# Kernel tuning notes

Measured on AMD Instinct MI355X. Metric: run time of the kernel, lower is better.

The kernel has to match this reference:

```python
import jax, jax.numpy as jnp
import numpy as np

SEQ, BATCH, HIDDEN = 4096, 16, 512


def setup_inputs() -> dict:
    key = jax.random.key(0)
    ks = jax.random.split(key, 8)
    scale = 1.0 / np.sqrt(HIDDEN)
    outputs_hidden = jax.random.normal(ks[0], (1, BATCH, HIDDEN), jnp.float32)
    encoder_out = jax.random.normal(ks[1], (SEQ, BATCH, HIDDEN), jnp.float32)
    encoder_features = jax.random.normal(ks[2], (SEQ, BATCH, HIDDEN), jnp.float32)
    # binary-ish float mask, mostly ones
    encoder_mask = (jax.random.uniform(ks[3], (BATCH, 1, SEQ)) > 0.1).astype(jnp.float32)
    # running sum of positive exp-scores; keep strictly positive
    temporal_scores_sum = jax.random.uniform(ks[4], (BATCH, 1, SEQ)) + 0.5
    W_feat = jax.random.normal(ks[5], (HIDDEN, HIDDEN), jnp.float32) * scale
    b_feat = jax.random.normal(ks[6], (HIDDEN,), jnp.float32)
    v_attn = jax.random.normal(ks[7], (HIDDEN,), jnp.float32) * scale
    return {
        "outputs_hidden": outputs_hidden,
        "encoder_out": encoder_out,
        "encoder_features": encoder_features,
        "encoder_mask": encoder_mask,
        "temporal_scores_sum": temporal_scores_sum,
        "W_feat": W_feat,
        "b_feat": b_feat,
        "v_attn": v_attn,
    }


def reference(outputs_hidden, encoder_out, encoder_features, encoder_mask,
              temporal_scores_sum, W_feat, b_feat, v_attn):
    # self.features: Linear(hidden, hidden) on decoder state [1, b, h]
    decoder_features = jnp.einsum('obh,kh->obk', outputs_hidden, W_feat) + b_feat
    # additive score: tanh(dec + enc) . v  -> [s, b]
    scores = jnp.einsum('sbh,h->sb', jnp.tanh(decoder_features + encoder_features), v_attn)
    # Permute(1,2,0) of [s,b,1] -> [b,1,s], then exp
    temporal_attention = jnp.exp(scores).T[:, None, :]  # [b, 1, s]
    attention = temporal_attention / temporal_scores_sum
    new_scores_sum = temporal_attention + temporal_scores_sum
    attention = attention * encoder_mask
    attention = attention / jnp.sum(attention, axis=-1, keepdims=True)  # Normalize(-1)
    enc = jnp.transpose(encoder_out, (1, 0, 2))           # [b, s, h]
    context = jnp.matmul(attention, enc)                  # [b, 1, h]
    context = jnp.transpose(context, (1, 0, 2))           # [1, b, h]
    return context, attention, new_scores_sum
```

## Files before the change

kernel.cpp:

```cpp
#include <hip/hip_runtime.h>
#include <hip/hip_bf16.h>
#include <stdint.h>

#define SEQ 4096
#define BATCH 16
#define HID 512
#define ATT_OFF (BATCH * HID)
#define NSS_OFF (BATCH * HID + BATCH * SEQ)
#define SPB 16
#define NCHUNK (SEQ / SPB)
#define SPW (SPB / 4)

typedef unsigned short u16;
typedef unsigned int u32;

__device__ __forceinline__ float bflo(u32 w) { return __uint_as_float(w << 16); }
__device__ __forceinline__ float bfhi(u32 w) { return __uint_as_float(w & 0xffff0000u); }

__device__ __forceinline__ u16 f2bf(float f) {
  u32 u = __float_as_uint(f);
  return (u16)((u + 0x7fffu + ((u >> 16) & 1u)) >> 16);
}

__device__ __forceinline__ int probe_bf16(const void* tssp) {
  const u16* t = (const u16*)tssp;
  int ok = 1;
  #pragma unroll
  for (int i = 0; i < 8; i += 2) {
    u16 u = t[i];
    ok &= (u >= 0x3F00 && u <= 0x3FC0) ? 1 : 0;
  }
  return ok;
}

template <int BF>
__device__ __forceinline__ float ld1(const void* p, size_t i) {
  if (BF) return __uint_as_float(((u32)((const u16*)p)[i]) << 16);
  return ((const float*)p)[i];
}

template <int BF>
__device__ __forceinline__ void st1(void* p, size_t i, float v) {
  if (BF) ((u16*)p)[i] = f2bf(v);
  else    ((float*)p)[i] = v;
}

template <int BF>
__device__ __forceinline__ void load8(const void* p, size_t e, float* o) {
  if (BF) {
    uint4 v = *(const uint4*)((const u16*)p + e);
    o[0]=bflo(v.x); o[1]=bfhi(v.x); o[2]=bflo(v.y); o[3]=bfhi(v.y);
    o[4]=bflo(v.z); o[5]=bfhi(v.z); o[6]=bflo(v.w); o[7]=bfhi(v.w);
  } else {
    const float4* f = (const float4*)((const float*)p + e);
    float4 a = f[0], b = f[1];
    o[0]=a.x; o[1]=a.y; o[2]=a.z; o[3]=a.w;
    o[4]=b.x; o[5]=b.y; o[6]=b.z; o[7]=b.w;
  }
}

__device__ __forceinline__ float fast_tanh(float x) {
  float e = __expf(2.0f * x);
  return 1.0f - 2.0f * __builtin_amdgcn_rcpf(e + 1.0f);
}

template <int BF>
__device__ __forceinline__ void k_dec_body(
    const void* oh, const void* W, const void* bias, float* dec) {
  int tid = threadIdx.x;
  int gw = blockIdx.x * 4 + (tid >> 6);
  int lane = tid & 63;
  int k = gw & (HID - 1);
  int b = gw >> 9;
  float wv[8], ov[8];
  load8<BF>(W,  (size_t)k * HID + lane * 8, wv);
  load8<BF>(oh, (size_t)b * HID + lane * 8, ov);
  float acc = 0.0f;
  #pragma unroll
  for (int j = 0; j < 8; ++j) acc += wv[j] * ov[j];
  #pragma unroll
  for (int off = 32; off; off >>= 1) acc += __shfl_xor(acc, off, 64);
  if (lane == 0) dec[b * HID + k] = acc + ld1<BF>(bias, k);
}

__global__ __launch_bounds__(256) void k_dec(
    const void* oh, const void* W, const void* bias, const void* tss,
    float* dec, float* denom) {
  if (blockIdx.x == 0 && threadIdx.x < BATCH) denom[threadIdx.x] = 0.0f;
  if (probe_bf16(tss)) k_dec_body<1>(oh, W, bias, dec);
  else                 k_dec_body<0>(oh, W, bias, dec);
}

template <int BF>
__device__ __forceinline__ void k_scores_body(
    const void* ef, const void* maskp, const void* tssp, const void* vp,
    const float* dec, float* w_buf, float* denom, void* out) {
  int tid = threadIdx.x, lane = tid & 63, wave = tid >> 6;
  int blk = blockIdx.x;
  int b = blk & (BATCH - 1);
  int chunk = blk >> 4;
  int s0 = chunk * SPB + wave * SPW;

  float ev[SPW][8];
  #pragma unroll
  for (int i = 0; i < SPW; ++i)
    load8<BF>(ef, ((size_t)(s0 + i) * BATCH + b) * HID + lane * 8, ev[i]);

  float dv[8], vv[8];
  #pragma unroll
  for (int j = 0; j < 8; ++j) dv[j] = dec[b * HID + lane * 8 + j];
  load8<BF>(vp, lane * 8, vv);

  float acc[SPW];
  #pragma unroll
  for (int i = 0; i < SPW; ++i) {
    float s = 0.0f;
    #pragma unroll
    for (int j = 0; j < 8; ++j) s += fast_tanh(ev[i][j] + dv[j]) * vv[j];
    acc[i] = s;
  }
  #pragma unroll
  for (int off = 32; off; off >>= 1) {
    #pragma unroll
    for (int i = 0; i < SPW; ++i) acc[i] += __shfl_xor(acc[i], off, 64);
  }
  float wsum = 0.0f;
  #pragma unroll
  for (int i = 0; i < SPW; ++i) {
    int s = s0 + i;
    float p  = __expf(acc[i]);
    float ts = ld1<BF>(tssp,  b * SEQ + s);
    float m  = ld1<BF>(maskp, b * SEQ + s);
    float wv = p * m * __builtin_amdgcn_rcpf(ts);
    wsum += wv;
    if (lane == 0) {
      st1<BF>(out, NSS_OFF + b * SEQ + s, p + ts);
      w_buf[b * SEQ + s] = wv;
    }
  }
  __shared__ float wpart[4];
  if (lane == 0) wpart[wave] = wsum;
  __syncthreads();
  if (tid == 0)
    atomicAdd(&denom[b], wpart[0] + wpart[1] + wpart[2] + wpart[3]);
}

__global__ __launch_bounds__(256, 4) void k_scores(
    const void* ef, const void* maskp, const void* tssp, const void* vp,
    const float* dec, float* w_buf, float* denom, void* out) {
  if (probe_bf16(tssp))
    k_scores_body<1>(ef, maskp, tssp, vp, dec, w_buf, denom, out);
  else
    k_scores_body<0>(ef, maskp, tssp, vp, dec, w_buf, denom, out);
}

template <int BF>
__device__ __forceinline__ void k_ctx_body(
    const void* eo, const float* w_buf, float* partial) {
  int tid = threadIdx.x, lane = tid & 63, wave = tid >> 6;
  int blk = blockIdx.x;
  int b = blk & (BATCH - 1);
  int chunk = blk >> 4;
  int s0 = chunk * SPB + wave * SPW;

  float eov[SPW][8];
  #pragma unroll
  for (int i = 0; i < SPW; ++i)
    load8<BF>(eo, ((size_t)(s0 + i) * BATCH + b) * HID + lane * 8, eov[i]);

  float w[SPW];
  #pragma unroll
  for (int i = 0; i < SPW; ++i) w[i] = w_buf[b * SEQ + s0 + i];

  float a[8] = {0,0,0,0,0,0,0,0};
  #pragma unroll
  for (int i = 0; i < SPW; ++i)
    #pragma unroll
    for (int j = 0; j < 8; ++j) a[j] += w[i] * eov[i][j];

  __shared__ float red[3 * 8 * 64];
  if (wave > 0) {
    #pragma unroll
    for (int j = 0; j < 8; ++j) red[((wave - 1) * 8 + j) * 64 + lane] = a[j];
  }
  __syncthreads();
  if (wave == 0) {
    #pragma unroll
    for (int k = 0; k < 3; ++k)
      #pragma unroll
      for (int j = 0; j < 8; ++j) a[j] += red[(k * 8 + j) * 64 + lane];
    float4* p4 = (float4*)(partial + ((size_t)b * NCHUNK + chunk) * HID + lane * 8);
    p4[0] = make_float4(a[0], a[1], a[2], a[3]);
    p4[1] = make_float4(a[4], a[5], a[6], a[7]);
  }
}

__global__ __launch_bounds__(256, 4) void k_ctx(
    const void* eo, const void* tssp, const float* w_buf, float* partial) {
  if (probe_bf16(tssp)) k_ctx_body<1>(eo, w_buf, partial);
  else                  k_ctx_body<0>(eo, w_buf, partial);
}

template <int BF>
__device__ __forceinline__ void k_fin_body(
    const float* w_buf, const float* denom, const float* partial, void* out) {
  int b = blockIdx.x >> 5;
  int part = blockIdx.x & 31;
  int t = threadIdx.x;
  float inv_d = __builtin_amdgcn_rcpf(denom[b]);
  if (t < 128) {
    int s = part * 128 + t;
    st1<BF>(out, ATT_OFF + b * SEQ + s, w_buf[b * SEQ + s] * inv_d);
  }
  int hl = t >> 4, cp = t & 15;
  int h = part * 16 + hl;
  float sum = 0.0f;
  #pragma unroll
  for (int c = cp; c < NCHUNK; c += 16)
    sum += partial[((size_t)b * NCHUNK + c) * HID + h];
  #pragma unroll
  for (int off = 8; off; off >>= 1) sum += __shfl_xor(sum, off, 64);
  if (cp == 0) st1<BF>(out, b * HID + h, sum * inv_d);
}

__global__ __launch_bounds__(256) void k_finalize(
    const float* w_buf, const float* denom, const float* partial,
    const void* tssp, void* out) {
  if (probe_bf16(tssp)) k_fin_body<1>(w_buf, denom, partial, out);
  else                  k_fin_body<0>(w_buf, denom, partial, out);
}

extern "C" void kernel_launch(void* const* d_in, const int* in_sizes, int n_in,
                              void* d_out, int out_size, void* d_ws, size_t ws_size,
                              hipStream_t stream) {
  const void* oh   = d_in[0];
  const void* eo   = d_in[1];
  const void* ef   = d_in[2];
  const void* mask = d_in[3];
  const void* tss  = d_in[4];
  const void* W    = d_in[5];
  const void* bias = d_in[6];
  const void* v    = d_in[7];

  float* ws      = (float*)d_ws;
  float* dec     = ws;
  float* w_buf   = dec + BATCH * HID;
  float* denom   = w_buf + BATCH * SEQ;
  float* partial = denom + 16;

  k_dec     <<<2048, 256, 0, stream>>>(oh, W, bias, tss, dec, denom);
  k_scores  <<<4096, 256, 0, stream>>>(ef, mask, tss, v, dec, w_buf, denom, d_out);
  k_ctx     <<<4096, 256, 0, stream>>>(eo, tss, w_buf, partial);
  k_finalize<<< 512, 256, 0, stream>>>(w_buf, denom, partial, tss, d_out);
}
```

Before: 322.4 us.

## Software-pipeline streaming kernels with double-buffered tiles and fewer, larger blocks

The scores and context kernels now have each wave handle four tiles of four sequence positions, using two register buffers. The next tile's loads are issued before the current tile is computed, so memory latency overlaps with compute. The grid shrinks fourfold, which means fewer atomics on the denominator and fewer partial rows for finalize to reduce. The cost is higher register pressure, so occupancy is lowered to 3 blocks per SIMD, and there are fewer blocks available to hide latency.

```diff
diff --git a/kernel.cpp b/kernel.cpp
--- a/kernel.cpp
+++ b/kernel.cpp
@@ -7,9 +7,12 @@
 #define HID 512
 #define ATT_OFF (BATCH * HID)
 #define NSS_OFF (BATCH * HID + BATCH * SEQ)
-#define SPB 16
-#define NCHUNK (SEQ / SPB)
-#define SPW (SPB / 4)
+
+#define SPW 4
+#define NT 4
+#define SBLK (4 * NT * SPW)
+#define NGRP (SEQ / SBLK)
+#define NSTREAM_BLOCKS (BATCH * NGRP)
 
 typedef unsigned short u16;
 typedef unsigned int u32;
@@ -98,46 +101,64 @@
   int tid = threadIdx.x, lane = tid & 63, wave = tid >> 6;
   int blk = blockIdx.x;
   int b = blk & (BATCH - 1);
-  int chunk = blk >> 4;
-  int s0 = chunk * SPB + wave * SPW;
-
-  float ev[SPW][8];
-  #pragma unroll
-  for (int i = 0; i < SPW; ++i)
-    load8<BF>(ef, ((size_t)(s0 + i) * BATCH + b) * HID + lane * 8, ev[i]);
+  int grp = blk >> 4;
+  int sw = grp * SBLK + wave * (NT * SPW);
 
   float dv[8], vv[8];
   #pragma unroll
   for (int j = 0; j < 8; ++j) dv[j] = dec[b * HID + lane * 8 + j];
   load8<BF>(vp, lane * 8, vv);
 
-  float acc[SPW];
-  #pragma unroll
-  for (int i = 0; i < SPW; ++i) {
-    float s = 0.0f;
-    #pragma unroll
-    for (int j = 0; j < 8; ++j) s += fast_tanh(ev[i][j] + dv[j]) * vv[j];
-    acc[i] = s;
-  }
-  #pragma unroll
-  for (int off = 32; off; off >>= 1) {
-    #pragma unroll
-    for (int i = 0; i < SPW; ++i) acc[i] += __shfl_xor(acc[i], off, 64);
-  }
+  float evA[SPW][8], evB[SPW][8];
+  float tsA[SPW], tsB[SPW], mA[SPW], mB[SPW];
   float wsum = 0.0f;
-  #pragma unroll
-  for (int i = 0; i < SPW; ++i) {
-    int s = s0 + i;
-    float p  = __expf(acc[i]);
-    float ts = ld1<BF>(tssp,  b * SEQ + s);
-    float m  = ld1<BF>(maskp, b * SEQ + s);
-    float wv = p * m * __builtin_amdgcn_rcpf(ts);
-    wsum += wv;
-    if (lane == 0) {
-      st1<BF>(out, NSS_OFF + b * SEQ + s, p + ts);
-      w_buf[b * SEQ + s] = wv;
-    }
-  }
+
+  auto LOADT = [&](float (&buf)[SPW][8], float (&ts)[SPW], float (&m)[SPW],
+                   int t) {
+    int s0 = sw + t * SPW;
+    #pragma unroll
+    for (int i = 0; i < SPW; ++i)
+      load8<BF>(ef, ((size_t)(s0 + i) * BATCH + b) * HID + lane * 8, buf[i]);
+    #pragma unroll
+    for (int i = 0; i < SPW; ++i) {
+      ts[i] = ld1<BF>(tssp,  b * SEQ + s0 + i);
+      m[i]  = ld1<BF>(maskp, b * SEQ + s0 + i);
+    }
+  };
+  auto COMP = [&](float (&buf)[SPW][8], float (&ts)[SPW], float (&m)[SPW],
+                  int t) {
+    int s0 = sw + t * SPW;
+    float acc[SPW];
+    #pragma unroll
+    for (int i = 0; i < SPW; ++i) {
+      float s = 0.0f;
+      #pragma unroll
+      for (int j = 0; j < 8; ++j) s += fast_tanh(buf[i][j] + dv[j]) * vv[j];
+      acc[i] = s;
+    }
+    #pragma unroll
+    for (int off = 32; off; off >>= 1) {
+      #pragma unroll
+      for (int i = 0; i < SPW; ++i) acc[i] += __shfl_xor(acc[i], off, 64);
+    }
+    #pragma unroll
+    for (int i = 0; i < SPW; ++i) {
+      float p  = __expf(acc[i]);
+      float wv = p * m[i] * __builtin_amdgcn_rcpf(ts[i]);
+      wsum += wv;
+      if (lane == 0) {
+        st1<BF>(out, NSS_OFF + b * SEQ + s0 + i, p + ts[i]);
+        w_buf[b * SEQ + s0 + i] = wv;
+      }
+    }
+  };
+
+  LOADT(evA, tsA, mA, 0);
+  LOADT(evB, tsB, mB, 1);  COMP(evA, tsA, mA, 0);
+  LOADT(evA, tsA, mA, 2);  COMP(evB, tsB, mB, 1);
+  LOADT(evB, tsB, mB, 3);  COMP(evA, tsA, mA, 2);
+                           COMP(evB, tsB, mB, 3);
+
   __shared__ float wpart[4];
   if (lane == 0) wpart[wave] = wsum;
   __syncthreads();
@@ -145,7 +166,7 @@
     atomicAdd(&denom[b], wpart[0] + wpart[1] + wpart[2] + wpart[3]);
 }
 
-__global__ __launch_bounds__(256, 4) void k_scores(
+__global__ __launch_bounds__(256, 3) void k_scores(
     const void* ef, const void* maskp, const void* tssp, const void* vp,
     const float* dec, float* w_buf, float* denom, void* out) {
   if (probe_bf16(tssp))
@@ -160,23 +181,33 @@
   int tid = threadIdx.x, lane = tid & 63, wave = tid >> 6;
   int blk = blockIdx.x;
   int b = blk & (BATCH - 1);
-  int chunk = blk >> 4;
-  int s0 = chunk * SPB + wave * SPW;
-
-  float eov[SPW][8];
-  #pragma unroll
-  for (int i = 0; i < SPW; ++i)
-    load8<BF>(eo, ((size_t)(s0 + i) * BATCH + b) * HID + lane * 8, eov[i]);
-
-  float w[SPW];
-  #pragma unroll
-  for (int i = 0; i < SPW; ++i) w[i] = w_buf[b * SEQ + s0 + i];
-
+  int grp = blk >> 4;
+  int sw = grp * SBLK + wave * (NT * SPW);
+
+  float eoA[SPW][8], eoB[SPW][8];
+  float wA[SPW], wB[SPW];
   float a[8] = {0,0,0,0,0,0,0,0};
-  #pragma unroll
-  for (int i = 0; i < SPW; ++i)
-    #pragma unroll
-    for (int j = 0; j < 8; ++j) a[j] += w[i] * eov[i][j];
+
+  auto LOADT = [&](float (&buf)[SPW][8], float (&w)[SPW], int t) {
+    int s0 = sw + t * SPW;
+    #pragma unroll
+    for (int i = 0; i < SPW; ++i)
+      load8<BF>(eo, ((size_t)(s0 + i) * BATCH + b) * HID + lane * 8, buf[i]);
+    #pragma unroll
+    for (int i = 0; i < SPW; ++i) w[i] = w_buf[b * SEQ + s0 + i];
+  };
+  auto COMP = [&](float (&buf)[SPW][8], float (&w)[SPW]) {
+    #pragma unroll
+    for (int i = 0; i < SPW; ++i)
+      #pragma unroll
+      for (int j = 0; j < 8; ++j) a[j] += w[i] * buf[i][j];
+  };
+
+  LOADT(eoA, wA, 0);
+  LOADT(eoB, wB, 1);  COMP(eoA, wA);
+  LOADT(eoA, wA, 2);  COMP(eoB, wB);
+  LOADT(eoB, wB, 3);  COMP(eoA, wA);
+                      COMP(eoB, wB);
 
   __shared__ float red[3 * 8 * 64];
   if (wave > 0) {
@@ -189,13 +220,13 @@
     for (int k = 0; k < 3; ++k)
       #pragma unroll
       for (int j = 0; j < 8; ++j) a[j] += red[(k * 8 + j) * 64 + lane];
-    float4* p4 = (float4*)(partial + ((size_t)b * NCHUNK + chunk) * HID + lane * 8);
+    float4* p4 = (float4*)(partial + ((size_t)b * NGRP + grp) * HID + lane * 8);
     p4[0] = make_float4(a[0], a[1], a[2], a[3]);
     p4[1] = make_float4(a[4], a[5], a[6], a[7]);
   }
 }
 
-__global__ __launch_bounds__(256, 4) void k_ctx(
+__global__ __launch_bounds__(256, 3) void k_ctx(
     const void* eo, const void* tssp, const float* w_buf, float* partial) {
   if (probe_bf16(tssp)) k_ctx_body<1>(eo, w_buf, partial);
   else                  k_ctx_body<0>(eo, w_buf, partial);
@@ -216,8 +247,8 @@
   int h = part * 16 + hl;
   float sum = 0.0f;
   #pragma unroll
-  for (int c = cp; c < NCHUNK; c += 16)
-    sum += partial[((size_t)b * NCHUNK + c) * HID + h];
+  for (int c = cp; c < NGRP; c += 16)
+    sum += partial[((size_t)b * NGRP + c) * HID + h];
   #pragma unroll
   for (int off = 8; off; off >>= 1) sum += __shfl_xor(sum, off, 64);
   if (cp == 0) st1<BF>(out, b * HID + h, sum * inv_d);
@@ -249,7 +280,8 @@
   float* partial = denom + 16;
 
   k_dec     <<<2048, 256, 0, stream>>>(oh, W, bias, tss, dec, denom);
-  k_scores  <<<4096, 256, 0, stream>>>(ef, mask, tss, v, dec, w_buf, denom, d_out);
-  k_ctx     <<<4096, 256, 0, stream>>>(eo, tss, w_buf, partial);
+  k_scores  <<<NSTREAM_BLOCKS, 256, 0, stream>>>(ef, mask, tss, v, dec, w_buf,
+                                                 denom, d_out);
+  k_ctx     <<<NSTREAM_BLOCKS, 256, 0, stream>>>(eo, tss, w_buf, partial);
   k_finalize<<< 512, 256, 0, stream>>>(w_buf, denom, partial, tss, d_out);
 }
```

After: 303.9 us. 1.06x faster.
